# Performance work log

Hardware: AMD Instinct MI355X
Metric: run time of the kernel (lower is better)

Reference implementation:

```python
import jax, jax.numpy as jnp
import numpy as np

NUM_EDGE_CLASS = 4
NODE_DIM = 64
BATCH = 32
NUM_NODES = 1024


def setup_inputs() -> dict:
    key = jax.random.key(0)
    k1, k2, k3, k4, k5 = jax.random.split(key, 5)
    node_state = jax.random.normal(k1, (BATCH, NUM_NODES, NODE_DIM), dtype=jnp.float32)
    adj_mat = jax.random.randint(k2, (BATCH, NUM_NODES, NUM_NODES), 0, NUM_EDGE_CLASS, dtype=jnp.int32)
    matrix_in = jax.random.normal(k3, (NUM_EDGE_CLASS, NODE_DIM, NODE_DIM), dtype=jnp.float32) * 0.1
    matrix_out = jax.random.normal(k4, (NUM_EDGE_CLASS, NODE_DIM, NODE_DIM), dtype=jnp.float32) * 0.1
    bias = jax.random.normal(k5, (2 * NODE_DIM,), dtype=jnp.float32)
    return {"node_state": node_state, "adj_mat": adj_mat,
            "matrix_in": matrix_in, "matrix_out": matrix_out, "bias": bias}


def reference(node_state, adj_mat, matrix_in, matrix_out, bias):
    """GGNN message passing (Li et al. Eq. 2).

    Original TF code builds a [b, n*d, n*d] block matrix where block (i, j)
    is matrix_in[adj_mat[b, i, j]] (and matrix_out[adj_mat[b, j, i]] for the
    outgoing direction), then matmuls against flattened node states. The
    equivalent fused math is:
      m_in[b,i]  = sum_j matrix_in[adj[b,i,j]]  @ h[b,j]
      m_out[b,i] = sum_j matrix_out[adj[b,j,i]] @ h[b,j]
    Implemented via a one-hot over the (small) set of edge classes so the
    per-edge d x d matrices are never materialized per edge.
    """
    h = node_state  # [b, n, d]
    onehot = jax.nn.one_hot(adj_mat, NUM_EDGE_CLASS, dtype=h.dtype)  # [b, n, n, c]
    # per-class neighbor aggregation, then one small matmul per class
    s_in = jnp.einsum('bijc,bje->bice', onehot, h)          # [b, n, c, d]
    m_in = jnp.einsum('bice,cde->bid', s_in, matrix_in)      # [b, n, d]
    s_out = jnp.einsum('bjic,bje->bice', onehot, h)          # transposed adjacency
    m_out = jnp.einsum('bice,cde->bid', s_out, matrix_out)   # [b, n, d]
    message = jnp.concatenate([m_in, m_out], axis=-1) + bias  # [b, n, 2d]
    return message
```

## Files before the change

### kernel.cpp

```cpp
#include <hip/hip_runtime.h>


namespace {

typedef unsigned short u16;
typedef __attribute__((ext_vector_type(8))) short bf16x8;
typedef __attribute__((ext_vector_type(4))) float f32x4;

constexpr int NB = 32;
constexpr int NN = 1024;
constexpr int ND = 64;

__device__ inline u16 f2bf(float x) {
    unsigned u = __float_as_uint(x);
    return (u16)((u + 0x7FFFu + ((u >> 16) & 1u)) >> 16);
}
__device__ inline unsigned pack2(int a, int b, int c) {
    return ((a == c) ? 0x3F80u : 0u) | ((b == c) ? 0x3F800000u : 0u);
}

__global__ __launch_bounds__(256) void prep(
    const float* __restrict__ h, const float* __restrict__ Min,
    const float* __restrict__ Mout, u16* __restrict__ Mws,
    u16* __restrict__ Hws)
{
    __shared__ u16 hT[64][72];
    const int t = threadIdx.x;
    const int bid = blockIdx.x;
    if (bid < 512) {
        const int b = bid >> 4, j0 = (bid & 15) << 6;
        const float* hb = h + ((size_t)b * NN + j0) * ND;
        #pragma unroll
        for (int k = 0; k < 4; ++k) {
            int idx = t + 256 * k;
            int j = idx >> 4, eq = idx & 15;
            float4 v = *(const float4*)(hb + j * ND + 4 * eq);
            hT[4 * eq + 0][j] = f2bf(v.x);
            hT[4 * eq + 1][j] = f2bf(v.y);
            hT[4 * eq + 2][j] = f2bf(v.z);
            hT[4 * eq + 3][j] = f2bf(v.w);
        }
        __syncthreads();
        #pragma unroll
        for (int k = 0; k < 2; ++k) {
            int idx = t + 256 * k;
            int e = idx >> 3, j8 = idx & 7;
            int4 v = *(const int4*)&hT[e][8 * j8];
            *(int4*)(Hws + ((size_t)b * 64 + e) * NN + j0 + 8 * j8) = v;
        }
    } else {
        const int base = (bid - 512) * 4096;
        #pragma unroll
        for (int k = 0; k < 16; ++k) {
            int idx = base + t + 256 * k;
            float v = (idx < 16384) ? Min[idx] : Mout[idx - 16384];
            Mws[idx] = f2bf(v);
        }
    }
}

__global__ __launch_bounds__(256) void ggnn_main(
    const int* __restrict__ adj, const float* __restrict__ bias,
    const u16* __restrict__ Mws, const u16* __restrict__ Hws,
    float* __restrict__ out)
{
    __shared__ __align__(16) char smem[36864];
    int (*adjt)[68]     = (int(*)[68])smem;
    u16 (*hT)[72]       = (u16(*)[72])(smem + 17408);
    u16 (*Sb)[16][72]   = (u16(*)[16][72])smem;

    const int t  = threadIdx.x;
    const int w  = t >> 6;
    const int ln = t & 15;
    const int qd = (t & 63) >> 4;
    const bool is_out = blockIdx.x >= 512;
    const int bid2 = blockIdx.x & 511;
    const int b  = bid2 >> 4;
    const int i0 = (bid2 & 15) << 6;

    const int* adjb  = adj + (size_t)b * NN * NN;
    const u16* Hb    = Hws + (size_t)b * 64 * NN;
    const u16* Mbase = Mws + (is_out ? 16384 : 0);
    const int  dofs  = is_out ? 64 : 0;

    f32x4 acc[4][4];
    #pragma unroll
    for (int c = 0; c < 4; ++c)
        #pragma unroll
        for (int nt = 0; nt < 4; ++nt) acc[c][nt] = (f32x4){0.f, 0.f, 0.f, 0.f};

    for (int j0 = 0; j0 < NN; j0 += 64) {
        __syncthreads();
        if (!is_out) {
            #pragma unroll
            for (int k = 0; k < 4; ++k) {
                int idx = t + 256 * k;
                int i = idx >> 4, j4 = idx & 15;
                int4 v = *(const int4*)(adjb + (size_t)(i0 + i) * NN + j0 + 4 * j4);
                *(int4*)&adjt[i][4 * j4] = v;
            }
        } else {
            #pragma unroll
            for (int k = 0; k < 4; ++k) {
                int idx = t + 256 * k;
                int jj = idx >> 4, i4 = idx & 15;
                int4 v = *(const int4*)(adjb + (size_t)(j0 + jj) * NN + i0 + 4 * i4);
                adjt[4 * i4 + 0][jj] = v.x;
                adjt[4 * i4 + 1][jj] = v.y;
                adjt[4 * i4 + 2][jj] = v.z;
                adjt[4 * i4 + 3][jj] = v.w;
            }
        }
        #pragma unroll
        for (int k = 0; k < 2; ++k) {
            int idx = t + 256 * k;
            int e = idx >> 3, j8 = idx & 7;
            int4 v = *(const int4*)(Hb + (size_t)e * NN + j0 + 8 * j8);
            *(int4*)&hT[e][8 * j8] = v;
        }
        __syncthreads();

        #pragma unroll
        for (int ks = 0; ks < 2; ++ks) {
            bf16x8 bf[4];
            #pragma unroll
            for (int nt = 0; nt < 4; ++nt)
                bf[nt] = *(const bf16x8*)&hT[nt * 16 + ln][ks * 32 + qd * 8];
            int4 aA = *(const int4*)&adjt[w * 16 + ln][ks * 32 + qd * 8];
            int4 aB = *(const int4*)&adjt[w * 16 + ln][ks * 32 + qd * 8 + 4];
            #pragma unroll
            for (int c = 0; c < 4; ++c) {
                union { unsigned u[4]; bf16x8 f; } x;
                x.u[0] = pack2(aA.x, aA.y, c);
                x.u[1] = pack2(aA.z, aA.w, c);
                x.u[2] = pack2(aB.x, aB.y, c);
                x.u[3] = pack2(aB.z, aB.w, c);
                #pragma unroll
                for (int nt = 0; nt < 4; ++nt)
                    acc[c][nt] = __builtin_amdgcn_mfma_f32_16x16x32_bf16(
                        x.f, bf[nt], acc[c][nt], 0, 0, 0);
            }
        }
    }

    __syncthreads();

    #pragma unroll
    for (int c = 0; c < 4; ++c)
        #pragma unroll
        for (int nt = 0; nt < 4; ++nt)
            #pragma unroll
            for (int r = 0; r < 4; ++r)
                Sb[w * 4 + c][qd * 4 + r][nt * 16 + ln] = f2bf(acc[c][nt][r]);

    f32x4 acc2[4];
    #pragma unroll
    for (int dt = 0; dt < 4; ++dt) {
        float bv = bias[dofs + dt * 16 + ln];
        acc2[dt] = (f32x4){bv, bv, bv, bv};
    }
    #pragma unroll
    for (int c = 0; c < 4; ++c) {
        #pragma unroll
        for (int ks2 = 0; ks2 < 2; ++ks2) {
            bf16x8 af = *(const bf16x8*)&Sb[w * 4 + c][ln][ks2 * 32 + qd * 8];
            #pragma unroll
            for (int dt = 0; dt < 4; ++dt) {
                bf16x8 mf = *(const bf16x8*)(Mbase
                    + (size_t)(c * 64 + dt * 16 + ln) * 64 + ks2 * 32 + qd * 8);
                acc2[dt] = __builtin_amdgcn_mfma_f32_16x16x32_bf16(
                    af, mf, acc2[dt], 0, 0, 0);
            }
        }
    }
    #pragma unroll
    for (int dt = 0; dt < 4; ++dt)
        #pragma unroll
        for (int r = 0; r < 4; ++r)
            out[((size_t)b * NN + i0 + w * 16 + qd * 4 + r) * 128
                + dofs + dt * 16 + ln] = acc2[dt][r];
}

}

extern "C" void kernel_launch(void* const* d_in, const int* in_sizes, int n_in,
                              void* d_out, int out_size, void* d_ws, size_t ws_size,
                              hipStream_t stream) {
    (void)in_sizes; (void)n_in; (void)out_size; (void)ws_size;
    const float* h    = (const float*)d_in[0];
    const int*   adj  = (const int*)d_in[1];
    const float* Min  = (const float*)d_in[2];
    const float* Mout = (const float*)d_in[3];
    const float* bias = (const float*)d_in[4];
    float* out = (float*)d_out;

    u16* Mws = (u16*)d_ws;
    u16* Hws = (u16*)((char*)d_ws + 65536);

    prep<<<520, 256, 0, stream>>>(h, Min, Mout, Mws, Hws);
    ggnn_main<<<1024, 256, 0, stream>>>(adj, bias, Mws, Hws, out);
}
```

Before: 276.4 us.

## Pack adjacency to 2-bit codes and use bit-plane basis to cut class matmuls

Adds a pre-pass that reads the int32 adjacency once and packs it into 2-bit codes, in both row and transposed layouts. Both directions then read the compact form through async global-to-LDS copies, so the main kernel no longer reads the adjacency twice as int32 and no longer does an LDS transpose. The four one-hot class matrices are re-expressed as bit-plane indicators (bit0, bit1, bit0&bit1) plus an all-ones term, which drops the MFMA aggregation work from four classes to three. The all-ones term is folded into a per-batch bias built from column sums of h. This adds extra kernels, atomics and a larger workspace, and rounding to bf16 with differenced matrices may change numerical error.

```diff
diff --git a/kernel.cpp b/kernel.cpp
--- a/kernel.cpp
+++ b/kernel.cpp
@@ -3,142 +3,213 @@
 
 namespace {
 
+typedef unsigned int  u32;
 typedef unsigned short u16;
 typedef __attribute__((ext_vector_type(8))) short bf16x8;
 typedef __attribute__((ext_vector_type(4))) float f32x4;
 
-constexpr int NB = 32;
 constexpr int NN = 1024;
 constexpr int ND = 64;
 
 __device__ inline u16 f2bf(float x) {
-    unsigned u = __float_as_uint(x);
+    u32 u = __float_as_uint(x);
     return (u16)((u + 0x7FFFu + ((u >> 16) & 1u)) >> 16);
 }
-__device__ inline unsigned pack2(int a, int b, int c) {
-    return ((a == c) ? 0x3F80u : 0u) | ((b == c) ? 0x3F800000u : 0u);
-}
-
-__global__ __launch_bounds__(256) void prep(
-    const float* __restrict__ h, const float* __restrict__ Min,
-    const float* __restrict__ Mout, u16* __restrict__ Mws,
-    u16* __restrict__ Hws)
-{
-    __shared__ u16 hT[64][72];
+__device__ inline float bf2f(u16 x) { return __uint_as_float(((u32)x) << 16); }
+
+#if defined(__has_builtin)
+#if __has_builtin(__builtin_amdgcn_global_load_lds)
+#define HAVE_GLL 1
+#endif
+#endif
+
+__device__ inline void async_copy16(const void* g, void* l) {
+#ifdef HAVE_GLL
+    typedef __attribute__((address_space(1))) const u32 gu32;
+    typedef __attribute__((address_space(3))) u32 lu32;
+    __builtin_amdgcn_global_load_lds((gu32*)g, (lu32*)l, 16, 0, 0);
+#else
+    int lane = threadIdx.x & 63;
+    ((uint4*)l)[lane] = *(const uint4*)((const char*)g);
+#endif
+}
+
+__global__ __launch_bounds__(256) void pack_adj(
+    const int* __restrict__ adj, u32* __restrict__ adjP, u32* __restrict__ adjPT)
+{
+    __shared__ u32 rp[64][16];
     const int t = threadIdx.x;
     const int bid = blockIdx.x;
-    if (bid < 512) {
-        const int b = bid >> 4, j0 = (bid & 15) << 6;
-        const float* hb = h + ((size_t)b * NN + j0) * ND;
-        #pragma unroll
-        for (int k = 0; k < 4; ++k) {
-            int idx = t + 256 * k;
-            int j = idx >> 4, eq = idx & 15;
-            float4 v = *(const float4*)(hb + j * ND + 4 * eq);
-            hT[4 * eq + 0][j] = f2bf(v.x);
-            hT[4 * eq + 1][j] = f2bf(v.y);
-            hT[4 * eq + 2][j] = f2bf(v.z);
-            hT[4 * eq + 3][j] = f2bf(v.w);
-        }
+    const int b = bid >> 6, It = (bid >> 4) & 3, Jt = (bid >> 2) & 3, s = bid & 3;
+    const int* base = adj + ((size_t)b << 20) + (size_t)(It * 256 + s * 64) * NN + Jt * 256;
+
+    const int row = t >> 2, seg = t & 3;
+    const int* rptr = base + (size_t)row * NN + seg * 64;
+    u32 w[4];
+    #pragma unroll
+    for (int q = 0; q < 4; ++q) {
+        int4 v0 = *(const int4*)(rptr + q * 16 + 0);
+        int4 v1 = *(const int4*)(rptr + q * 16 + 4);
+        int4 v2 = *(const int4*)(rptr + q * 16 + 8);
+        int4 v3 = *(const int4*)(rptr + q * 16 + 12);
+        u32 u = (u32)(v0.x & 3) | ((u32)(v0.y & 3) << 2) | ((u32)(v0.z & 3) << 4) | ((u32)(v0.w & 3) << 6)
+              | ((u32)(v1.x & 3) << 8) | ((u32)(v1.y & 3) << 10) | ((u32)(v1.z & 3) << 12) | ((u32)(v1.w & 3) << 14)
+              | ((u32)(v2.x & 3) << 16) | ((u32)(v2.y & 3) << 18) | ((u32)(v2.z & 3) << 20) | ((u32)(v2.w & 3) << 22)
+              | ((u32)(v3.x & 3) << 24) | ((u32)(v3.y & 3) << 26) | ((u32)(v3.z & 3) << 28) | ((u32)(v3.w & 3) << 30);
+        w[q] = u;
+    }
+    u32* op = adjP + (((((size_t)b * 4 + Jt) * 16 + It * 4 + s) * 4 + seg) * 64 + row) * 4;
+    *(uint4*)op = make_uint4(w[0], w[1], w[2], w[3]);
+    *(uint4*)&rp[row][seg * 4] = make_uint4(w[0], w[1], w[2], w[3]);
+    __syncthreads();
+
+    const int sc = t >> 6, il = t & 63;
+    const int cw = sc * 4 + (il >> 4);
+    const int bp = (il & 15) * 2;
+    u32 o[4];
+    #pragma unroll
+    for (int jj = 0; jj < 4; ++jj) {
+        u32 acc = 0;
+        #pragma unroll
+        for (int k = 0; k < 16; ++k)
+            acc |= ((rp[jj * 16 + k][cw] >> bp) & 3u) << (2 * k);
+        o[jj] = acc;
+    }
+    u32* op2 = adjPT + (((((size_t)b * 4 + It) * 16 + Jt * 4 + sc) * 4 + s) * 64 + il) * 4;
+    *(uint4*)op2 = make_uint4(o[0], o[1], o[2], o[3]);
+}
+
+__global__ __launch_bounds__(256) void prep_h(
+    const float* __restrict__ h, u16* __restrict__ Hws, float* __restrict__ PA)
+{
+    __shared__ u16 hl[256][72];
+    const int t = threadIdx.x;
+    const int b = blockIdx.x >> 2, jc = blockIdx.x & 3;
+    const float* hb = h + ((size_t)b * NN + jc * 256) * ND;
+    #pragma unroll
+    for (int k = 0; k < 16; ++k) {
+        int j = k * 16 + (t >> 4);
+        int e4 = (t & 15) * 4;
+        float4 v = *(const float4*)(hb + (size_t)j * ND + e4);
+        *(u32*)&hl[j][e4]     = (u32)f2bf(v.x) | ((u32)f2bf(v.y) << 16);
+        *(u32*)&hl[j][e4 + 2] = (u32)f2bf(v.z) | ((u32)f2bf(v.w) << 16);
+    }
+    __syncthreads();
+    u16* ob = Hws + (size_t)(b * 4 + jc) * 2048 * 8;
+    const int e = t & 63;
+    float psum = 0.f;
+    #pragma unroll
+    for (int k = 0; k < 8; ++k) {
+        int u = k * 4 + (t >> 6);
+        u32 p0, p1, p2, p3;
+        u16 x0 = hl[u * 8 + 0][e], x1 = hl[u * 8 + 1][e], x2 = hl[u * 8 + 2][e], x3 = hl[u * 8 + 3][e];
+        u16 x4 = hl[u * 8 + 4][e], x5 = hl[u * 8 + 5][e], x6 = hl[u * 8 + 6][e], x7 = hl[u * 8 + 7][e];
+        psum += bf2f(x0) + bf2f(x1) + bf2f(x2) + bf2f(x3) + bf2f(x4) + bf2f(x5) + bf2f(x6) + bf2f(x7);
+        p0 = (u32)x0 | ((u32)x1 << 16); p1 = (u32)x2 | ((u32)x3 << 16);
+        p2 = (u32)x4 | ((u32)x5 << 16); p3 = (u32)x6 | ((u32)x7 << 16);
+        *(uint4*)(ob + (size_t)(u * 64 + e) * 8) = make_uint4(p0, p1, p2, p3);
+    }
+    atomicAdd(&PA[b * 64 + e], psum);
+}
+
+__global__ __launch_bounds__(256) void prep_m(
+    const float* __restrict__ Min, const float* __restrict__ Mout,
+    const float* __restrict__ bias, const float* __restrict__ PA,
+    u16* __restrict__ Mws, float* __restrict__ basews)
+{
+    const int t = threadIdx.x, bb = blockIdx.x;
+    if (bb == 0) {
+        for (int i = t; i < 2 * 4096; i += 256) {
+            const float* M = (i < 4096) ? Min : Mout;
+            int idx = i & 4095;
+            float m0 = M[idx], m1 = M[4096 + idx], m2 = M[8192 + idx], m3 = M[12288 + idx];
+            u16* o = Mws + (size_t)(i >> 12) * 3 * 4096;
+            o[idx]            = f2bf(m1 - m0);
+            o[4096 + idx]     = f2bf(m2 - m0);
+            o[8192 + idx]     = f2bf(m0 - m1 - m2 + m3);
+        }
+    }
+    if (t < 128) {
+        int d = t & 63, dir = t >> 6;
+        const float* M0 = (dir ? Mout : Min) + d * 64;
+        float s = bias[dir * 64 + d];
+        #pragma unroll 8
+        for (int e = 0; e < 64; ++e) s += PA[bb * 64 + e] * M0[e];
+        basews[(bb * 2 + dir) * 64 + d] = s;
+    }
+}
+
+__global__ __launch_bounds__(256, 4) void ggnn_main(
+    const u32* __restrict__ adjP, const u32* __restrict__ adjPT,
+    const u16* __restrict__ Hws, const u16* __restrict__ Mws,
+    const float* __restrict__ basews, float* __restrict__ out)
+{
+    __shared__ __align__(16) char smem[36864];
+    char* adjL = smem;
+    char* hL   = smem + 4096;
+    u16 (*Sb)[16][72] = (u16(*)[16][72])smem;
+
+    const int t = threadIdx.x;
+    const int w = t >> 6, lane = t & 63;
+    const int ln = t & 15, qd = (t & 63) >> 4, qd2 = qd >> 1;
+    const int shamt = (qd & 1) * 16;
+    const int bid = blockIdx.x;
+    const int dir = bid >> 9;
+    const int b = (bid >> 4) & 31, it = bid & 15;
+
+    const u32* Adir = dir ? adjPT : adjP;
+    f32x4 acc[3][4];
+    #pragma unroll
+    for (int p = 0; p < 3; ++p)
+        #pragma unroll
+        for (int nt = 0; nt < 4; ++nt) acc[p][nt] = (f32x4){0.f, 0.f, 0.f, 0.f};
+
+    for (int jc = 0; jc < 4; ++jc) {
         __syncthreads();
-        #pragma unroll
-        for (int k = 0; k < 2; ++k) {
-            int idx = t + 256 * k;
-            int e = idx >> 3, j8 = idx & 7;
-            int4 v = *(const int4*)&hT[e][8 * j8];
-            *(int4*)(Hws + ((size_t)b * 64 + e) * NN + j0 + 8 * j8) = v;
-        }
-    } else {
-        const int base = (bid - 512) * 4096;
-        #pragma unroll
-        for (int k = 0; k < 16; ++k) {
-            int idx = base + t + 256 * k;
-            float v = (idx < 16384) ? Min[idx] : Mout[idx - 16384];
-            Mws[idx] = f2bf(v);
-        }
-    }
-}
-
-__global__ __launch_bounds__(256) void ggnn_main(
-    const int* __restrict__ adj, const float* __restrict__ bias,
-    const u16* __restrict__ Mws, const u16* __restrict__ Hws,
-    float* __restrict__ out)
-{
-    __shared__ __align__(16) char smem[36864];
-    int (*adjt)[68]     = (int(*)[68])smem;
-    u16 (*hT)[72]       = (u16(*)[72])(smem + 17408);
-    u16 (*Sb)[16][72]   = (u16(*)[16][72])smem;
-
-    const int t  = threadIdx.x;
-    const int w  = t >> 6;
-    const int ln = t & 15;
-    const int qd = (t & 63) >> 4;
-    const bool is_out = blockIdx.x >= 512;
-    const int bid2 = blockIdx.x & 511;
-    const int b  = bid2 >> 4;
-    const int i0 = (bid2 & 15) << 6;
-
-    const int* adjb  = adj + (size_t)b * NN * NN;
-    const u16* Hb    = Hws + (size_t)b * 64 * NN;
-    const u16* Mbase = Mws + (is_out ? 16384 : 0);
-    const int  dofs  = is_out ? 64 : 0;
-
-    f32x4 acc[4][4];
-    #pragma unroll
-    for (int c = 0; c < 4; ++c)
-        #pragma unroll
-        for (int nt = 0; nt < 4; ++nt) acc[c][nt] = (f32x4){0.f, 0.f, 0.f, 0.f};
-
-    for (int j0 = 0; j0 < NN; j0 += 64) {
+        const char* at = (const char*)(Adir + (size_t)((b * 4 + jc) * 16 + it) * 1024);
+        const char* ht = (const char*)(Hws + (size_t)(b * 4 + jc) * 16384);
+        if (w == 0) {
+            #pragma unroll
+            for (int u = 0; u < 4; ++u)
+                async_copy16(at + u * 1024 + lane * 16, adjL + u * 1024);
+        }
+        #pragma unroll
+        for (int k = 0; k < 8; ++k) {
+            int i = w + k * 4;
+            async_copy16(ht + i * 1024 + lane * 16, hL + i * 1024);
+        }
         __syncthreads();
-        if (!is_out) {
-            #pragma unroll
-            for (int k = 0; k < 4; ++k) {
-                int idx = t + 256 * k;
-                int i = idx >> 4, j4 = idx & 15;
-                int4 v = *(const int4*)(adjb + (size_t)(i0 + i) * NN + j0 + 4 * j4);
-                *(int4*)&adjt[i][4 * j4] = v;
-            }
-        } else {
-            #pragma unroll
-            for (int k = 0; k < 4; ++k) {
-                int idx = t + 256 * k;
-                int jj = idx >> 4, i4 = idx & 15;
-                int4 v = *(const int4*)(adjb + (size_t)(j0 + jj) * NN + i0 + 4 * i4);
-                adjt[4 * i4 + 0][jj] = v.x;
-                adjt[4 * i4 + 1][jj] = v.y;
-                adjt[4 * i4 + 2][jj] = v.z;
-                adjt[4 * i4 + 3][jj] = v.w;
-            }
-        }
-        #pragma unroll
-        for (int k = 0; k < 2; ++k) {
-            int idx = t + 256 * k;
-            int e = idx >> 3, j8 = idx & 7;
-            int4 v = *(const int4*)(Hb + (size_t)e * NN + j0 + 8 * j8);
-            *(int4*)&hT[e][8 * j8] = v;
-        }
-        __syncthreads();
-
-        #pragma unroll
-        for (int ks = 0; ks < 2; ++ks) {
+
+        uint4 Ar[4];
+        #pragma unroll
+        for (int u = 0; u < 4; ++u)
+            Ar[u] = *(const uint4*)(adjL + (u * 64 + w * 16 + ln) * 16);
+
+        #pragma unroll
+        for (int ks = 0; ks < 8; ++ks) {
+            uint4 Q = Ar[ks >> 1];
+            u32 a = (ks & 1) ? (qd2 ? Q.w : Q.z) : (qd2 ? Q.y : Q.x);
+            u32 f  = (a >> shamt) & 0xFFFFu;
+            u32 x0 = f & 0x5555u;
+            u32 x1 = (f >> 1) & 0x5555u;
+            u32 xt = x0 & x1;
             bf16x8 bf[4];
             #pragma unroll
             for (int nt = 0; nt < 4; ++nt)
-                bf[nt] = *(const bf16x8*)&hT[nt * 16 + ln][ks * 32 + qd * 8];
-            int4 aA = *(const int4*)&adjt[w * 16 + ln][ks * 32 + qd * 8];
-            int4 aB = *(const int4*)&adjt[w * 16 + ln][ks * 32 + qd * 8 + 4];
-            #pragma unroll
-            for (int c = 0; c < 4; ++c) {
-                union { unsigned u[4]; bf16x8 f; } x;
-                x.u[0] = pack2(aA.x, aA.y, c);
-                x.u[1] = pack2(aA.z, aA.w, c);
-                x.u[2] = pack2(aB.x, aB.y, c);
-                x.u[3] = pack2(aB.z, aB.w, c);
+                bf[nt] = *(const bf16x8*)(hL + ((ks * 4 + qd) * 64 + nt * 16 + ln) * 16);
+            #pragma unroll
+            for (int p = 0; p < 3; ++p) {
+                u32 xp = (p == 0) ? x0 : (p == 1) ? x1 : xt;
+                union { u32 u[4]; bf16x8 v; } A;
+                #pragma unroll
+                for (int wd = 0; wd < 4; ++wd) {
+                    u32 z = xp >> (4 * wd);
+                    A.u[wd] = ((z & 1u) | ((z & 4u) << 14)) * 0x3F80u;
+                }
                 #pragma unroll
                 for (int nt = 0; nt < 4; ++nt)
-                    acc[c][nt] = __builtin_amdgcn_mfma_f32_16x16x32_bf16(
-                        x.f, bf[nt], acc[c][nt], 0, 0, 0);
+                    acc[p][nt] = __builtin_amdgcn_mfma_f32_16x16x32_bf16(
+                        A.v, bf[nt], acc[p][nt], 0, 0, 0);
             }
         }
     }
@@ -146,30 +217,31 @@
     __syncthreads();
 
     #pragma unroll
-    for (int c = 0; c < 4; ++c)
+    for (int p = 0; p < 3; ++p)
         #pragma unroll
         for (int nt = 0; nt < 4; ++nt)
             #pragma unroll
             for (int r = 0; r < 4; ++r)
-                Sb[w * 4 + c][qd * 4 + r][nt * 16 + ln] = f2bf(acc[c][nt][r]);
-
+                Sb[w * 3 + p][qd * 4 + r][nt * 16 + ln] = f2bf(acc[p][nt][r]);
+
+    const float* bv = basews + (b * 2 + dir) * 64;
     f32x4 acc2[4];
     #pragma unroll
     for (int dt = 0; dt < 4; ++dt) {
-        float bv = bias[dofs + dt * 16 + ln];
-        acc2[dt] = (f32x4){bv, bv, bv, bv};
-    }
-    #pragma unroll
-    for (int c = 0; c < 4; ++c) {
+        float v = bv[dt * 16 + ln];
+        acc2[dt] = (f32x4){v, v, v, v};
+    }
+    const u16* Mb = Mws + (size_t)dir * 3 * 4096;
+    #pragma unroll
+    for (int p = 0; p < 3; ++p) {
         #pragma unroll
         for (int ks2 = 0; ks2 < 2; ++ks2) {
-            bf16x8 af = *(const bf16x8*)&Sb[w * 4 + c][ln][ks2 * 32 + qd * 8];
+            bf16x8 af = *(const bf16x8*)&Sb[w * 3 + p][ln][ks2 * 32 + qd * 8];
             #pragma unroll
             for (int dt = 0; dt < 4; ++dt) {
-                bf16x8 mf = *(const bf16x8*)(Mbase
-                    + (size_t)(c * 64 + dt * 16 + ln) * 64 + ks2 * 32 + qd * 8);
-                acc2[dt] = __builtin_amdgcn_mfma_f32_16x16x32_bf16(
-                    af, mf, acc2[dt], 0, 0, 0);
+                bf16x8 mf = *(const bf16x8*)(Mb + (size_t)(p * 64 + dt * 16 + ln) * 64
+                                             + ks2 * 32 + qd * 8);
+                acc2[dt] = __builtin_amdgcn_mfma_f32_16x16x32_bf16(af, mf, acc2[dt], 0, 0, 0);
             }
         }
     }
@@ -177,8 +249,8 @@
     for (int dt = 0; dt < 4; ++dt)
         #pragma unroll
         for (int r = 0; r < 4; ++r)
-            out[((size_t)b * NN + i0 + w * 16 + qd * 4 + r) * 128
-                + dofs + dt * 16 + ln] = acc2[dt][r];
+            out[((size_t)b * NN + it * 64 + w * 16 + qd * 4 + r) * 128
+                + dir * 64 + dt * 16 + ln] = acc2[dt][r];
 }
 
 }
@@ -194,9 +266,17 @@
     const float* bias = (const float*)d_in[4];
     float* out = (float*)d_out;
 
-    u16* Mws = (u16*)d_ws;
-    u16* Hws = (u16*)((char*)d_ws + 65536);
-
-    prep<<<520, 256, 0, stream>>>(h, Min, Mout, Mws, Hws);
-    ggnn_main<<<1024, 256, 0, stream>>>(adj, bias, Mws, Hws, out);
-}
+    char* ws = (char*)d_ws;
+    u32* adjP   = (u32*)(ws + 0);
+    u32* adjPT  = (u32*)(ws + 8388608);
+    u16* Hws    = (u16*)(ws + 16777216);
+    float* PA   = (float*)(ws + 20971520);
+    u16* Mws    = (u16*)(ws + 20979712);
+    float* basews = (float*)(ws + 21028864);
+
+    hipMemsetAsync(PA, 0, 32 * 64 * sizeof(float), stream);
+    pack_adj<<<2048, 256, 0, stream>>>(adj, adjP, adjPT);
+    prep_h<<<128, 256, 0, stream>>>(h, Hws, PA);
+    prep_m<<<32, 256, 0, stream>>>(Min, Mout, bias, PA, Mws, basews);
+    ggnn_main<<<1024, 256, 0, stream>>>(adjP, adjPT, Hws, Mws, basews, out);
+}
```

New measurement: 262.1 us. 1.05x faster.
